# Optimization experiments

Measured on AMD Instinct MI355X. Metric: run time of the kernel, lower is better.

Reference implementation:

```python
import jax, jax.numpy as jnp
import numpy as np


def setup_inputs() -> dict:
    key = jax.random.key(0)
    k1, k2 = jax.random.split(key)
    B, H, W, E = 8, 32, 32, 256   # latent grid (NHWC layout, as in vector_quantize)
    N_E = 16384                   # codebook size
    x = jax.random.normal(k1, (B, H, W, E), dtype=jnp.float32)
    codebook = jax.random.normal(k2, (N_E, E), dtype=jnp.float32)
    return {"x": x, "codebook": codebook}


def reference(x, codebook):
    # d[b,h,w,k] = ||x[b,h,w] - codebook[k]||^2 (expanded form, as in source)
    x_sq = jnp.sum(x * x, axis=-1, keepdims=True)            # [B,H,W,1]
    cb_sq = jnp.sum(codebook * codebook, axis=1)              # [N_E]
    cross = jnp.einsum('bhwe,ke->bhwk', x, codebook)          # [B,H,W,N_E]
    d = x_sq + cb_sq - 2.0 * cross
    indices = jnp.argmin(d, axis=-1)                          # [B,H,W]
    x_q = jnp.take(codebook, indices, axis=0)                 # one-hot @ codebook == row gather
    # straight-through / ReplaceGrad: forward value is x_q, gradient flows to x
    return x + jax.lax.stop_gradient(x_q - x)
```

## Files before the change

### kernel.cpp

```cpp
#include <hip/hip_runtime.h>
#include <stdint.h>

#define M_PIX 8192
#define N_CB  16384
#define KD    256

typedef float f32x4 __attribute__((ext_vector_type(4)));
typedef int   i32x4 __attribute__((ext_vector_type(4)));
typedef int   i32x8 __attribute__((ext_vector_type(8)));
typedef unsigned long long ull;

#define OFF_CF8  (0ULL)
#define OFF_XF8  (4ULL << 20)
#define OFF_CBSQ (6ULL << 20)
#define OFF_SLOT (7ULL << 20)
#define WS_REQ   (15ULL << 20)

__device__ __forceinline__ unsigned int fkey(float s) {
  unsigned int f = __float_as_uint(s);
  return f ^ ((unsigned int)(((int)f) >> 31) | 0x80000000u);
}
__device__ __forceinline__ unsigned char f2e4m3(float v) {
  float av = fminf(fabsf(v), 448.0f);
  const unsigned s = (__float_as_uint(v) >> 24) & 0x80u;
  unsigned m;
  if (av >= 0.015625f) {
    unsigned u = __float_as_uint(av);
    u += 0x7FFFFu + ((u >> 20) & 1u);
    m = (((u >> 23) - 120u) << 3) | ((u >> 20) & 7u);
  } else {
    m = (unsigned)(int)rintf(av * 512.0f);
  }
  return (unsigned char)(s | m);
}
__device__ __forceinline__ void gl_lds16(const unsigned char* g, char* l) {
  __builtin_amdgcn_global_load_lds(
      (const __attribute__((address_space(1))) unsigned int*)(const void*)g,
      (__attribute__((address_space(3))) unsigned int*)(void*)l,
      16, 0, 0);
}
__device__ __forceinline__ void merge2(float p, float q, float& v1, float& v2) {
  const float M = fmaxf(v1, p);
  v1 = fminf(v1, p);
  v2 = fminf(fminf(v2, q), M);
}
__device__ __forceinline__ i32x8 ld32(const char* p, int addr) {
  const i32x4 lo = *(const i32x4*)(const void*)(p + addr);
  const i32x4 hi = *(const i32x4*)(const void*)(p + (addr ^ 16));
  return (i32x8){lo.x, lo.y, lo.z, lo.w, hi.x, hi.y, hi.z, hi.w};
}

__global__ __launch_bounds__(256) void prep_kernel(
    const float* __restrict__ x, const float* __restrict__ cb,
    unsigned char* __restrict__ Cf8, unsigned char* __restrict__ Xf8,
    float* __restrict__ cbsq) {
  const int wid = threadIdx.x >> 6, lane = threadIdx.x & 63;
  const int row = blockIdx.x * 4 + wid;
  const bool isCb = (row < N_CB);
  const int rowL = isCb ? row : row - N_CB;
  const float* src = (isCb ? cb : x) + (size_t)rowL * KD;
  const float4 v = ((const float4*)src)[lane];
  uchar4 pk;
  pk.x = f2e4m3(v.x); pk.y = f2e4m3(v.y); pk.z = f2e4m3(v.z); pk.w = f2e4m3(v.w);
  *(uchar4*)(void*)((isCb ? Cf8 : Xf8) + (size_t)rowL * KD + lane * 4) = pk;
  if (isCb) {
    float ss = v.x*v.x + v.y*v.y + v.z*v.z + v.w*v.w;
    #pragma unroll
    for (int off = 32; off > 0; off >>= 1) ss += __shfl_xor(ss, off);
    if (lane == 0) cbsq[rowL] = ss;
  }
}


__global__ __launch_bounds__(256, 3) void gemm_top2_kernel(
    const unsigned char* __restrict__ Xf8, const unsigned char* __restrict__ Cf8,
    const float* __restrict__ cbsq, float2* __restrict__ slots) {
  __shared__ __align__(16) char smem[36864];
  char* A_s = smem;
  char* B_s = smem + 16384;
  float* v1p = (float*)smem;
  float* v2p = (float*)(smem + 18432);

  const int tid = threadIdx.x;
  const int wid = tid >> 6, lane = tid & 63;
  const int wy = wid >> 1, wx = wid & 1;
  const int q = lane >> 4, c = lane & 15;

  const int bx = blockIdx.x & 7, bg = blockIdx.x >> 3;
  const int mt = bg >> 4;
  const int nt = bx * 16 + (bg & 15);
  const int m0 = mt * 128, n0 = nt * 128;

  const int swz = (c & 7) << 4;
  int aaddr[4], baddr[4];
  #pragma unroll
  for (int i = 0; i < 4; i++) {
    aaddr[i] = (((wy * 64 + i * 16 + c) * 128) + q * 32) ^ swz;
    baddr[i] = ((((wx * 64 + i * 16 + c) * 128) + q * 32) ^ swz) + 16384;
  }

  const f32x4 zf = {0.f, 0.f, 0.f, 0.f};
  f32x4 acc[4][4];
  #pragma unroll
  for (int i = 0; i < 4; i++)
    #pragma unroll
    for (int j = 0; j < 4; j++) acc[i][j] = zf;

  const int srow8 = lane >> 3;
  const int sgb = ((lane & 7) ^ srow8) * 16;

  #pragma unroll
  for (int j = 0; j < 4; j++) {
    const int chunk = j * 4 + wid;
    const int row = chunk * 8 + srow8;
    gl_lds16(Xf8 + (size_t)(m0 + row) * KD + sgb, A_s + chunk * 1024);
    gl_lds16(Cf8 + (size_t)(n0 + row) * KD + sgb, B_s + chunk * 1024);
  }
  __syncthreads();

  i32x8 af0[4], bf0[4];
  #pragma unroll
  for (int mi = 0; mi < 4; mi++) af0[mi] = ld32(smem, aaddr[mi]);
  #pragma unroll
  for (int ni = 0; ni < 4; ni++) bf0[ni] = ld32(smem, baddr[ni]);
  __builtin_amdgcn_sched_barrier(0);
  __syncthreads();

  #pragma unroll
  for (int j = 0; j < 4; j++) {
    const int chunk = j * 4 + wid;
    const int row = chunk * 8 + srow8;
    gl_lds16(Xf8 + (size_t)(m0 + row) * KD + sgb + 128, A_s + chunk * 1024);
    gl_lds16(Cf8 + (size_t)(n0 + row) * KD + sgb + 128, B_s + chunk * 1024);
  }
  __builtin_amdgcn_sched_barrier(0);

  #pragma unroll
  for (int mi = 0; mi < 4; mi++)
    #pragma unroll
    for (int ni = 0; ni < 4; ni++)
      acc[mi][ni] = __builtin_amdgcn_mfma_scale_f32_16x16x128_f8f6f4(
          af0[mi], bf0[ni], acc[mi][ni], 0, 0,
          0, 0x7F7F7F7F,
          0, 0x7F7F7F7F);
  __builtin_amdgcn_sched_barrier(0);
  __syncthreads();

  float cs[4]; unsigned colp[4];
  #pragma unroll
  for (int ni = 0; ni < 4; ni++) {
    colp[ni] = wx * 64 + ni * 16 + c;
    cs[ni] = cbsq[n0 + colp[ni]];
  }

  #pragma unroll
  for (int mi = 0; mi < 4; mi++) af0[mi] = ld32(smem, aaddr[mi]);
  #pragma unroll
  for (int ni = 0; ni < 4; ni++) bf0[ni] = ld32(smem, baddr[ni]);
  __builtin_amdgcn_sched_barrier(0);
  __syncthreads();

  #pragma unroll
  for (int mi = 0; mi < 4; mi++)
    #pragma unroll
    for (int ni = 0; ni < 4; ni++)
      acc[mi][ni] = __builtin_amdgcn_mfma_scale_f32_16x16x128_f8f6f4(
          af0[mi], bf0[ni], acc[mi][ni], 0, 0,
          0, 0x7F7F7F7F, 0, 0x7F7F7F7F);

  const float FINF = __uint_as_float(0x7F800000u);

  #pragma unroll
  for (int mi = 0; mi < 4; mi++) {
    #pragma unroll
    for (int r = 0; r < 4; r++) {
      float k[4];
      #pragma unroll
      for (int ni = 0; ni < 4; ni++) {
        const float s = fmaf(-2.f, acc[mi][ni][r], cs[ni]);
        k[ni] = __uint_as_float((__float_as_uint(s) & 0xFFFFFF80u) | colp[ni]);
      }
      const float m1 = fminf(k[0], k[1]), M1 = fmaxf(k[0], k[1]);
      const float m2 = fminf(k[2], k[3]), M2 = fmaxf(k[2], k[3]);
      const float v1 = fminf(m1, m2);
      const float v2 = fminf(fmaxf(m1, m2), fminf(M1, M2));
      const int row = wy * 64 + mi * 16 + q * 4 + r;
      const int slot = wx * 16 + c;
      v1p[row * 36 + slot] = v1;
      v2p[row * 36 + slot] = v2;
    }
  }
  __syncthreads();

  {
    const int srow = tid >> 1, half = tid & 1;
    float v1 = FINF, v2 = FINF;
    #pragma unroll
    for (int jj = 0; jj < 4; jj++) {
      const float4 a = *(const float4*)(const void*)(v1p + srow * 36 + half * 16 + jj * 4);
      const float4 b = *(const float4*)(const void*)(v2p + srow * 36 + half * 16 + jj * 4);
      merge2(a.x, b.x, v1, v2);
      merge2(a.y, b.y, v1, v2);
      merge2(a.z, b.z, v1, v2);
      merge2(a.w, b.w, v1, v2);
    }
    const float b1 = __shfl_xor(v1, 1), b2 = __shfl_xor(v2, 1);
    const float hi = fmaxf(v1, b1);
    v1 = fminf(v1, b1);
    v2 = fminf(fminf(v2, b2), hi);
    if (!half)
      slots[(size_t)nt * M_PIX + m0 + srow] = make_float2(v1, v2);
  }
}

__global__ __launch_bounds__(256) void reduce_rescore_gather(
    const float* __restrict__ x, const float* __restrict__ cb,
    const float* __restrict__ cbsq, const float2* __restrict__ slots,
    float* __restrict__ out) {
  const int wid = threadIdx.x >> 6, lane = threadIdx.x & 63;
  const int pixel = blockIdx.x * 4 + wid;
  const int g = lane >> 4, lg = lane & 15;

  const float2 sA = slots[(size_t)lane * M_PIX + pixel];
  const float2 sB = slots[(size_t)(64 + lane) * M_PIX + pixel];
  const float sc[4] = {sA.x, sA.y, sB.x, sB.y};
  float mn = fminf(fminf(sc[0], sc[1]), fminf(sc[2], sc[3]));
  #pragma unroll
  for (int off = 1; off < 64; off <<= 1) mn = fminf(mn, __shfl_xor(mn, off));
  const float thr = mn + 10.0f;

  float4 xv16[4];
  #pragma unroll
  for (int k = 0; k < 4; k++)
    xv16[k] = ((const float4*)x)[(size_t)pixel * 64 + lg * 4 + k];

  const float4 z4 = make_float4(0.f, 0.f, 0.f, 0.f);
  ull best = ~0ULL;
  float4 wc[4] = {z4, z4, z4, z4};

  #pragma unroll
  for (int j = 0; j < 4; j++) {
    ull mask = __ballot(sc[j] < thr);
    while (mask) {
      int mysrc = -1;
      #pragma unroll
      for (int gg = 0; gg < 4; gg++) {
        if (mask) {
          const int s = (int)__ffsll((long long)mask) - 1;
          mask &= mask - 1;
          if (gg == g) mysrc = s;
        }
      }
      const bool act = mysrc >= 0;
      const int srcs = act ? mysrc : 0;
      const float val = __shfl(sc[j], srcs);
      const unsigned ij = (unsigned)(((j >> 1) * 64 + srcs) * 128) +
                          (__float_as_uint(val) & 127u);
      float4 cv[4] = {z4, z4, z4, z4};
      float csq = 0.f;
      if (act) {
        #pragma unroll
        for (int k = 0; k < 4; k++)
          cv[k] = ((const float4*)cb)[(size_t)ij * 64 + lg * 4 + k];
        csq = cbsq[ij];
      }
      float d = cv[0].x*xv16[0].x + cv[0].y*xv16[0].y
              + cv[0].z*xv16[0].z + cv[0].w*xv16[0].w;
      d += cv[1].x*xv16[1].x + cv[1].y*xv16[1].y
         + cv[1].z*xv16[1].z + cv[1].w*xv16[1].w;
      d += cv[2].x*xv16[2].x + cv[2].y*xv16[2].y
         + cv[2].z*xv16[2].z + cv[2].w*xv16[2].w;
      d += cv[3].x*xv16[3].x + cv[3].y*xv16[3].y
         + cv[3].z*xv16[3].z + cv[3].w*xv16[3].w;
      #pragma unroll
      for (int off = 1; off < 16; off <<= 1) d += __shfl_xor(d, off);
      const float sv = fmaf(-2.f, d, csq);
      const ull key = act ? (((ull)fkey(sv) << 32) | ij) : ~0ULL;
      if (key < best) {
        best = key;
        wc[0] = cv[0]; wc[1] = cv[1]; wc[2] = cv[2]; wc[3] = cv[3];
      }
    }
  }

  ull gb = best;
  {
    const ull o1 = __shfl_xor(gb, 16); gb = o1 < gb ? o1 : gb;
    const ull o2 = __shfl_xor(gb, 32); gb = o2 < gb ? o2 : gb;
  }
  if (best == gb) {
    #pragma unroll
    for (int k = 0; k < 4; k++)
      ((float4*)out)[(size_t)pixel * 64 + lg * 4 + k] = wc[k];
  }
}

__global__ __launch_bounds__(256) void fallback_kernel(
    const float* __restrict__ x, const float* __restrict__ cb,
    float* __restrict__ out) {
  __shared__ float xs[256];
  __shared__ unsigned long long keys[4];
  __shared__ int widx;
  const int p = blockIdx.x;
  const int tid = threadIdx.x, wid = tid >> 6, lane = tid & 63;
  xs[tid] = x[(size_t)p * KD + tid];
  __syncthreads();
  const float4 xv = ((const float4*)xs)[lane];
  float bestS = 3.4e38f; int bestI = 0;
  for (int k = wid; k < N_CB; k += 4) {
    const float4 cv = ((const float4*)cb)[(size_t)k * 64 + lane];
    float t = cv.x*(cv.x - 2.f*xv.x) + cv.y*(cv.y - 2.f*xv.y)
            + cv.z*(cv.z - 2.f*xv.z) + cv.w*(cv.w - 2.f*xv.w);
    #pragma unroll
    for (int off = 1; off < 64; off <<= 1) t += __shfl_xor(t, off);
    if (t < bestS) { bestS = t; bestI = k; }
  }
  if (lane == 0)
    keys[wid] = ((unsigned long long)fkey(bestS) << 32) | (unsigned int)bestI;
  __syncthreads();
  if (tid == 0) {
    unsigned long long m = keys[0];
    for (int i = 1; i < 4; i++) if (keys[i] < m) m = keys[i];
    widx = (int)(unsigned int)(m & 0xFFFFFFFFULL);
  }
  __syncthreads();
  out[(size_t)p * KD + tid] = cb[(size_t)widx * KD + tid];
}

extern "C" void kernel_launch(void* const* d_in, const int* in_sizes, int n_in,
                              void* d_out, int out_size, void* d_ws, size_t ws_size,
                              hipStream_t stream) {
  const float* x  = (const float*)d_in[0];
  const float* cb = (const float*)d_in[1];
  float* out = (float*)d_out;

  if (ws_size < WS_REQ) {
    fallback_kernel<<<M_PIX, 256, 0, stream>>>(x, cb, out);
    return;
  }

  char* ws = (char*)d_ws;
  unsigned char* Cf8 = (unsigned char*)(ws + OFF_CF8);
  unsigned char* Xf8 = (unsigned char*)(ws + OFF_XF8);
  float* cbsq        = (float*)(ws + OFF_CBSQ);
  float2* slots      = (float2*)(ws + OFF_SLOT);

  prep_kernel<<<(N_CB + M_PIX) / 4, 256, 0, stream>>>(x, cb, Cf8, Xf8, cbsq);
  gemm_top2_kernel<<<M_PIX, 256, 0, stream>>>(Xf8, Cf8, cbsq, slots);
  reduce_rescore_gather<<<M_PIX / 4, 256, 0, stream>>>(x, cb, cbsq, slots, out);
}
```

Measured before the change: 136.9 us.

## Reuse X tile in registers across two codebook tiles per block

Each block now loads its 128-pixel X tile once, keeps both K-halves of its fragments in registers, and loops over two consecutive 128-code codebook tiles. The grid is halved and the block-to-tile mapping is rearranged to match. The aim is to cut redundant X loads and per-block launch and prologue overhead. In exchange it raises register pressure, lowers the occupancy hint from 3 to 2, and serializes the two tiles with extra barriers and less latency hiding.

```diff
diff --git a/kernel.cpp b/kernel.cpp
--- a/kernel.cpp
+++ b/kernel.cpp
@@ -72,7 +72,7 @@
 }
 
 
-__global__ __launch_bounds__(256, 3) void gemm_top2_kernel(
+__global__ __launch_bounds__(256, 2) void gemm_top2_kernel(
     const unsigned char* __restrict__ Xf8, const unsigned char* __restrict__ Cf8,
     const float* __restrict__ cbsq, float2* __restrict__ slots) {
   __shared__ __align__(16) char smem[36864];
@@ -87,24 +87,17 @@
   const int q = lane >> 4, c = lane & 15;
 
   const int bx = blockIdx.x & 7, bg = blockIdx.x >> 3;
-  const int mt = bg >> 4;
-  const int nt = bx * 16 + (bg & 15);
-  const int m0 = mt * 128, n0 = nt * 128;
+  const int mt  = bg >> 3;
+  const int nt0 = bx * 16 + (bg & 7) * 2;
+  const int m0  = mt * 128;
 
   const int swz = (c & 7) << 4;
   int aaddr[4], baddr[4];
   #pragma unroll
   for (int i = 0; i < 4; i++) {
     aaddr[i] = (((wy * 64 + i * 16 + c) * 128) + q * 32) ^ swz;
-    baddr[i] = ((((wx * 64 + i * 16 + c) * 128) + q * 32) ^ swz) + 16384;
-  }
-
-  const f32x4 zf = {0.f, 0.f, 0.f, 0.f};
-  f32x4 acc[4][4];
-  #pragma unroll
-  for (int i = 0; i < 4; i++)
-    #pragma unroll
-    for (int j = 0; j < 4; j++) acc[i][j] = zf;
+    baddr[i] = (((wx * 64 + i * 16 + c) * 128) + q * 32) ^ swz;
+  }
 
   const int srow8 = lane >> 3;
   const int sgb = ((lane & 7) ^ srow8) * 16;
@@ -113,103 +106,126 @@
   for (int j = 0; j < 4; j++) {
     const int chunk = j * 4 + wid;
     const int row = chunk * 8 + srow8;
-    gl_lds16(Xf8 + (size_t)(m0 + row) * KD + sgb, A_s + chunk * 1024);
-    gl_lds16(Cf8 + (size_t)(n0 + row) * KD + sgb, B_s + chunk * 1024);
-  }
-  __syncthreads();
-
-  i32x8 af0[4], bf0[4];
+    gl_lds16(Xf8 + (size_t)(m0 + row) * KD + sgb,       A_s + chunk * 1024);
+    gl_lds16(Xf8 + (size_t)(m0 + row) * KD + sgb + 128, B_s + chunk * 1024);
+  }
+  __syncthreads();
+
+  i32x8 af0[4], af1[4];
   #pragma unroll
   for (int mi = 0; mi < 4; mi++) af0[mi] = ld32(smem, aaddr[mi]);
   #pragma unroll
-  for (int ni = 0; ni < 4; ni++) bf0[ni] = ld32(smem, baddr[ni]);
+  for (int mi = 0; mi < 4; mi++) af1[mi] = ld32(smem, aaddr[mi] + 16384);
   __builtin_amdgcn_sched_barrier(0);
   __syncthreads();
 
-  #pragma unroll
-  for (int j = 0; j < 4; j++) {
-    const int chunk = j * 4 + wid;
-    const int row = chunk * 8 + srow8;
-    gl_lds16(Xf8 + (size_t)(m0 + row) * KD + sgb + 128, A_s + chunk * 1024);
-    gl_lds16(Cf8 + (size_t)(n0 + row) * KD + sgb + 128, B_s + chunk * 1024);
-  }
-  __builtin_amdgcn_sched_barrier(0);
-
-  #pragma unroll
-  for (int mi = 0; mi < 4; mi++)
-    #pragma unroll
-    for (int ni = 0; ni < 4; ni++)
-      acc[mi][ni] = __builtin_amdgcn_mfma_scale_f32_16x16x128_f8f6f4(
-          af0[mi], bf0[ni], acc[mi][ni], 0, 0,
-          0, 0x7F7F7F7F,
-          0, 0x7F7F7F7F);
-  __builtin_amdgcn_sched_barrier(0);
-  __syncthreads();
-
-  float cs[4]; unsigned colp[4];
-  #pragma unroll
-  for (int ni = 0; ni < 4; ni++) {
-    colp[ni] = wx * 64 + ni * 16 + c;
-    cs[ni] = cbsq[n0 + colp[ni]];
-  }
-
-  #pragma unroll
-  for (int mi = 0; mi < 4; mi++) af0[mi] = ld32(smem, aaddr[mi]);
-  #pragma unroll
-  for (int ni = 0; ni < 4; ni++) bf0[ni] = ld32(smem, baddr[ni]);
-  __builtin_amdgcn_sched_barrier(0);
-  __syncthreads();
-
-  #pragma unroll
-  for (int mi = 0; mi < 4; mi++)
-    #pragma unroll
-    for (int ni = 0; ni < 4; ni++)
-      acc[mi][ni] = __builtin_amdgcn_mfma_scale_f32_16x16x128_f8f6f4(
-          af0[mi], bf0[ni], acc[mi][ni], 0, 0,
-          0, 0x7F7F7F7F, 0, 0x7F7F7F7F);
-
   const float FINF = __uint_as_float(0x7F800000u);
-
-  #pragma unroll
-  for (int mi = 0; mi < 4; mi++) {
-    #pragma unroll
-    for (int r = 0; r < 4; r++) {
-      float k[4];
-      #pragma unroll
-      for (int ni = 0; ni < 4; ni++) {
-        const float s = fmaf(-2.f, acc[mi][ni][r], cs[ni]);
-        k[ni] = __uint_as_float((__float_as_uint(s) & 0xFFFFFF80u) | colp[ni]);
-      }
-      const float m1 = fminf(k[0], k[1]), M1 = fmaxf(k[0], k[1]);
-      const float m2 = fminf(k[2], k[3]), M2 = fmaxf(k[2], k[3]);
-      const float v1 = fminf(m1, m2);
-      const float v2 = fminf(fmaxf(m1, m2), fminf(M1, M2));
-      const int row = wy * 64 + mi * 16 + q * 4 + r;
-      const int slot = wx * 16 + c;
-      v1p[row * 36 + slot] = v1;
-      v2p[row * 36 + slot] = v2;
-    }
-  }
-  __syncthreads();
-
-  {
-    const int srow = tid >> 1, half = tid & 1;
-    float v1 = FINF, v2 = FINF;
-    #pragma unroll
-    for (int jj = 0; jj < 4; jj++) {
-      const float4 a = *(const float4*)(const void*)(v1p + srow * 36 + half * 16 + jj * 4);
-      const float4 b = *(const float4*)(const void*)(v2p + srow * 36 + half * 16 + jj * 4);
-      merge2(a.x, b.x, v1, v2);
-      merge2(a.y, b.y, v1, v2);
-      merge2(a.z, b.z, v1, v2);
-      merge2(a.w, b.w, v1, v2);
-    }
-    const float b1 = __shfl_xor(v1, 1), b2 = __shfl_xor(v2, 1);
-    const float hi = fmaxf(v1, b1);
-    v1 = fminf(v1, b1);
-    v2 = fminf(fminf(v2, b2), hi);
-    if (!half)
-      slots[(size_t)nt * M_PIX + m0 + srow] = make_float2(v1, v2);
+  const f32x4 zf = {0.f, 0.f, 0.f, 0.f};
+
+  #pragma unroll 1
+  for (int t = 0; t < 2; t++) {
+    const int nt = nt0 + t;
+    const int n0 = nt * 128;
+
+    #pragma unroll
+    for (int j = 0; j < 4; j++) {
+      const int chunk = j * 4 + wid;
+      const int row = chunk * 8 + srow8;
+      gl_lds16(Cf8 + (size_t)(n0 + row) * KD + sgb, A_s + chunk * 1024);
+    }
+    __syncthreads();
+
+    i32x8 bfr[4];
+    #pragma unroll
+    for (int ni = 0; ni < 4; ni++) bfr[ni] = ld32(smem, baddr[ni]);
+    __builtin_amdgcn_sched_barrier(0);
+
+    #pragma unroll
+    for (int j = 0; j < 4; j++) {
+      const int chunk = j * 4 + wid;
+      const int row = chunk * 8 + srow8;
+      gl_lds16(Cf8 + (size_t)(n0 + row) * KD + sgb + 128, B_s + chunk * 1024);
+    }
+    __builtin_amdgcn_sched_barrier(0);
+
+    f32x4 acc[4][4];
+    #pragma unroll
+    for (int i = 0; i < 4; i++)
+      #pragma unroll
+      for (int j = 0; j < 4; j++) acc[i][j] = zf;
+
+    #pragma unroll
+    for (int mi = 0; mi < 4; mi++)
+      #pragma unroll
+      for (int ni = 0; ni < 4; ni++)
+        acc[mi][ni] = __builtin_amdgcn_mfma_scale_f32_16x16x128_f8f6f4(
+            af0[mi], bfr[ni], acc[mi][ni], 0, 0,
+            0, 0x7F7F7F7F,
+            0, 0x7F7F7F7F);
+    __builtin_amdgcn_sched_barrier(0);
+    __syncthreads();
+
+    float cs[4]; unsigned colp[4];
+    #pragma unroll
+    for (int ni = 0; ni < 4; ni++) {
+      colp[ni] = wx * 64 + ni * 16 + c;
+      cs[ni] = cbsq[n0 + colp[ni]];
+    }
+    #pragma unroll
+    for (int ni = 0; ni < 4; ni++) bfr[ni] = ld32(smem, baddr[ni] + 16384);
+    __builtin_amdgcn_sched_barrier(0);
+    __syncthreads();
+
+    #pragma unroll
+    for (int mi = 0; mi < 4; mi++)
+      #pragma unroll
+      for (int ni = 0; ni < 4; ni++)
+        acc[mi][ni] = __builtin_amdgcn_mfma_scale_f32_16x16x128_f8f6f4(
+            af1[mi], bfr[ni], acc[mi][ni], 0, 0,
+            0, 0x7F7F7F7F, 0, 0x7F7F7F7F);
+
+    #pragma unroll
+    for (int mi = 0; mi < 4; mi++) {
+      #pragma unroll
+      for (int r = 0; r < 4; r++) {
+        float k[4];
+        #pragma unroll
+        for (int ni = 0; ni < 4; ni++) {
+          const float s = fmaf(-2.f, acc[mi][ni][r], cs[ni]);
+          k[ni] = __uint_as_float((__float_as_uint(s) & 0xFFFFFF80u) | colp[ni]);
+        }
+        const float m1 = fminf(k[0], k[1]), M1 = fmaxf(k[0], k[1]);
+        const float m2 = fminf(k[2], k[3]), M2 = fmaxf(k[2], k[3]);
+        const float v1 = fminf(m1, m2);
+        const float v2 = fminf(fmaxf(m1, m2), fminf(M1, M2));
+        const int row = wy * 64 + mi * 16 + q * 4 + r;
+        const int slot = wx * 16 + c;
+        v1p[row * 36 + slot] = v1;
+        v2p[row * 36 + slot] = v2;
+      }
+    }
+    __syncthreads();
+
+    {
+      const int srow = tid >> 1, half = tid & 1;
+      float v1 = FINF, v2 = FINF;
+      #pragma unroll
+      for (int jj = 0; jj < 4; jj++) {
+        const float4 a = *(const float4*)(const void*)(v1p + srow * 36 + half * 16 + jj * 4);
+        const float4 b = *(const float4*)(const void*)(v2p + srow * 36 + half * 16 + jj * 4);
+        merge2(a.x, b.x, v1, v2);
+        merge2(a.y, b.y, v1, v2);
+        merge2(a.z, b.z, v1, v2);
+        merge2(a.w, b.w, v1, v2);
+      }
+      const float b1 = __shfl_xor(v1, 1), b2 = __shfl_xor(v2, 1);
+      const float hi = fmaxf(v1, b1);
+      v1 = fminf(v1, b1);
+      v2 = fminf(fminf(v2, b2), hi);
+      if (!half)
+        slots[(size_t)nt * M_PIX + m0 + srow] = make_float2(v1, v2);
+    }
+    if (t == 0) __syncthreads();
   }
 }
 
@@ -346,6 +362,6 @@
   float2* slots      = (float2*)(ws + OFF_SLOT);
 
   prep_kernel<<<(N_CB + M_PIX) / 4, 256, 0, stream>>>(x, cb, Cf8, Xf8, cbsq);
-  gemm_top2_kernel<<<M_PIX, 256, 0, stream>>>(Xf8, Cf8, cbsq, slots);
+  gemm_top2_kernel<<<M_PIX / 2, 256, 0, stream>>>(Xf8, Cf8, cbsq, slots);
   reduce_rescore_gather<<<M_PIX / 4, 256, 0, stream>>>(x, cb, cbsq, slots, out);
 }
```

Result: slower. 141.4 us (+3.3%).
